# Optimization experiments

Measured on AMD Instinct MI355X. Metric: run time of the kernel, lower is better.

The kernel has to match this reference:

```python
import jax, jax.numpy as jnp
import numpy as np

B, Q, K, D, H = 2, 2048, 2048, 1024, 16
HD = D // H  # 64
EPS = 1e-6  # flax LayerNorm default epsilon


def setup_inputs() -> dict:
    key = jax.random.key(0)
    ks = jax.random.split(key, 12)
    s = 1.0 / np.sqrt(D)  # lecun_normal-like scale
    inputs_q = jax.random.normal(ks[0], (B, Q, D), jnp.float32)
    bias = jax.random.normal(ks[1], (B, 1, Q, K), jnp.float32)
    mask = jax.random.randint(ks[2], (B, 1, Q, K), 0, 2).astype(jnp.bool_)
    wq = jax.random.normal(ks[3], (D, H, HD), jnp.float32) * s
    wk = jax.random.normal(ks[4], (D, H, HD), jnp.float32) * s
    wv = jax.random.normal(ks[5], (D, H, HD), jnp.float32) * s
    bq = jnp.zeros((H, HD), jnp.float32)
    bk = jnp.zeros((H, HD), jnp.float32)
    bv = jnp.zeros((H, HD), jnp.float32)
    q_scale = jnp.ones((HD,), jnp.float32)
    k_scale = jnp.ones((HD,), jnp.float32)
    wo = jax.random.normal(ks[6], (H, HD, D), jnp.float32) * s
    bo = jnp.zeros((D,), jnp.float32)
    return dict(inputs_q=inputs_q, bias=bias, mask=mask, wq=wq, bq=bq,
                wk=wk, bk=bk, wv=wv, bv=bv, q_scale=q_scale, k_scale=k_scale,
                wo=wo, bo=bo)


def _layernorm_nobias(x, scale):
    # normalize over last axis (head_dim), no bias, like flax LayerNorm(use_bias=False)
    mean = jnp.mean(x, axis=-1, keepdims=True)
    var = jnp.mean(jnp.square(x - mean), axis=-1, keepdims=True)
    return (x - mean) * jax.lax.rsqrt(var + EPS) * scale


def reference(inputs_q, bias, mask, wq, bq, wk, bk, wv, bv, q_scale, k_scale, wo, bo):
    # QKV projections (self-attention: k and v inputs default to inputs_q)
    q = jnp.einsum('bqd,dhe->bqhe', inputs_q, wq) + bq  # [B,Q,H,HD]
    k = jnp.einsum('bkd,dhe->bkhe', inputs_q, wk) + bk  # [B,K,H,HD]
    v = jnp.einsum('bkd,dhe->bkhe', inputs_q, wv) + bv  # [B,K,H,HD]
    # optional QK layernorm (normalize_qk=True)
    q = _layernorm_nobias(q, q_scale)
    k = _layernorm_nobias(k, k_scale)
    # attention weights
    q = q / jnp.sqrt(jnp.asarray(q.shape[-1], q.dtype))
    attn = jnp.einsum('bqhe,bkhe->bhqk', q, k)  # [B,H,Q,K]
    attn = attn + bias
    big_neg = jnp.finfo(q.dtype).min
    attn = jnp.where(mask, attn, big_neg)
    attn = jax.nn.softmax(attn.astype(jnp.float32), axis=-1).astype(q.dtype)
    # weighted values + output projection
    x = jnp.einsum('bhqk,bkhe->bqhe', attn, v)  # [B,Q,H,HD]
    out = jnp.einsum('bqhe,heo->bqo', x, wo) + bo  # [B,Q,D]
    return out
```

## Files before the change

kernel.cpp:

```cpp
#include <hip/hip_runtime.h>
#include <cstdint>
#include <cstddef>

typedef __bf16 bf16_t;
typedef __bf16 bf16x8 __attribute__((ext_vector_type(8)));
typedef __bf16 bf16x4 __attribute__((ext_vector_type(4)));
typedef _Float16 f16_t;
typedef _Float16 f16x4 __attribute__((ext_vector_type(4)));
typedef float f32x4 __attribute__((ext_vector_type(4)));

constexpr int BB = 2, SS = 2048, DD = 1024, HH = 16, HDIM = 64;
constexpr int BS = BB * SS;
constexpr float LOG2E = 1.4426950408889634f;

__device__ __forceinline__ void glds16(const void* g, void* l) {
  __builtin_amdgcn_global_load_lds((const __attribute__((address_space(1))) void*)g,
                                   (__attribute__((address_space(3))) void*)l, 16, 0, 0);
}

__global__ __launch_bounds__(256) void prep_fused(
    const float* __restrict__ x, const float* __restrict__ wq, const float* __restrict__ wk,
    const float* __restrict__ wv, const float* __restrict__ wo, const float* __restrict__ bias,
    const int* __restrict__ mask, bf16_t* __restrict__ xb, bf16_t* __restrict__ wqkv_t,
    bf16_t* __restrict__ wo_t, bf16_t* __restrict__ bmq) {
  __shared__ float tile[64][65];
  int bid = blockIdx.x;
  int t = threadIdx.x;
  if (bid < 4096) {
    int i = bid * 256 + t;
    float4 v = ((const float4*)x)[i];
    union { bf16_t h[4]; uint2 u; } o;
    o.h[0] = (bf16_t)v.x; o.h[1] = (bf16_t)v.y; o.h[2] = (bf16_t)v.z; o.h[3] = (bf16_t)v.w;
    ((uint2*)xb)[i] = o.u;
  } else if (bid < 5120) {
    int id = bid - 4096;
    int which = id >> 8, tr = (id >> 4) & 15, tc = id & 15;
    const float* src = (which == 0) ? wq : (which == 1) ? wk : (which == 2) ? wv : wo;
    bf16_t* dst = (which < 3) ? wqkv_t : wo_t;
    int noff = (which < 3) ? which * 1024 : 0;
#pragma unroll
    for (int p = 0; p < 4; ++p) {
      int e = (p * 256 + t) * 4;
      int r = e >> 6, c = e & 63;
      float4 v = *(const float4*)&src[(size_t)(tr * 64 + r) * 1024 + tc * 64 + c];
      tile[r][c] = v.x; tile[r][c + 1] = v.y; tile[r][c + 2] = v.z; tile[r][c + 3] = v.w;
    }
    __syncthreads();
#pragma unroll
    for (int p = 0; p < 4; ++p) {
      int e = (p * 256 + t) * 4;
      int r = e >> 6, c = e & 63;
      union { bf16_t h[4]; uint2 u; } o;
#pragma unroll
      for (int j = 0; j < 4; ++j) o.h[j] = (bf16_t)tile[c + j][r];
      *(uint2*)&dst[(size_t)(noff + tc * 64 + r) * 1024 + tr * 64 + c] = o.u;
    }
  } else {
    int i = (bid - 5120) * 256 + t;
    float4 b0 = ((const float4*)bias)[i * 2];
    float4 b1 = ((const float4*)bias)[i * 2 + 1];
    int4 m0 = ((const int4*)mask)[i * 2];
    int4 m1 = ((const int4*)mask)[i * 2 + 1];
    union { bf16_t h[8]; uint4 u; } o;
    o.h[0] = (bf16_t)(m0.x ? b0.x * LOG2E - 8.0f : -2.0e38f);
    o.h[1] = (bf16_t)(m0.y ? b0.y * LOG2E - 8.0f : -2.0e38f);
    o.h[2] = (bf16_t)(m0.z ? b0.z * LOG2E - 8.0f : -2.0e38f);
    o.h[3] = (bf16_t)(m0.w ? b0.w * LOG2E - 8.0f : -2.0e38f);
    o.h[4] = (bf16_t)(m1.x ? b1.x * LOG2E - 8.0f : -2.0e38f);
    o.h[5] = (bf16_t)(m1.y ? b1.y * LOG2E - 8.0f : -2.0e38f);
    o.h[6] = (bf16_t)(m1.z ? b1.z * LOG2E - 8.0f : -2.0e38f);
    o.h[7] = (bf16_t)(m1.w ? b1.w * LOG2E - 8.0f : -2.0e38f);
    ((uint4*)bmq)[i] = o.u;
  }
}

template <bool OUT_F32>
__global__ __launch_bounds__(256) void gemm_bt(const bf16_t* __restrict__ A,
                                               const bf16_t* __restrict__ Bt,
                                               bf16_t* __restrict__ Cb, float* __restrict__ Cf,
                                               const float* __restrict__ bias, int M, int N,
                                               int Kd) {
  __shared__ __align__(16) bf16_t As[128][32];
  __shared__ __align__(16) bf16_t Bs[128][32];
  int tid = threadIdx.x;
  int lane = tid & 63, w = tid >> 6;
  int lo = lane & 15, quad = lane >> 4;
  int wm = w >> 1, wn = w & 1;
  int m0 = blockIdx.y * 128, n0 = blockIdx.x * 128;
  int srow = lane >> 2;
  int scol = (lane & 3) * 8;
  f32x4 acc[4][4] = {};
  for (int kk = 0; kk < Kd; kk += 32) {
#pragma unroll
    for (int t = 0; t < 2; ++t) {
      int rb = (w * 2 + t) * 16;
      glds16(&A[(size_t)(m0 + rb + srow) * Kd + kk + scol], &As[rb][0]);
      glds16(&Bt[(size_t)(n0 + rb + srow) * Kd + kk + scol], &Bs[rb][0]);
    }
    asm volatile("s_waitcnt vmcnt(0)" ::: "memory");
    __syncthreads();
    bf16x8 am[4], bn[4];
#pragma unroll
    for (int i = 0; i < 4; ++i) am[i] = *(const bf16x8*)&As[wm * 64 + i * 16 + lo][quad * 8];
#pragma unroll
    for (int i = 0; i < 4; ++i) bn[i] = *(const bf16x8*)&Bs[wn * 64 + i * 16 + lo][quad * 8];
#pragma unroll
    for (int mi = 0; mi < 4; ++mi)
#pragma unroll
      for (int ni = 0; ni < 4; ++ni)
        acc[mi][ni] = __builtin_amdgcn_mfma_f32_16x16x32_bf16(am[mi], bn[ni], acc[mi][ni], 0, 0, 0);
    __syncthreads();
  }
#pragma unroll
  for (int mi = 0; mi < 4; ++mi) {
#pragma unroll
    for (int ni = 0; ni < 4; ++ni) {
#pragma unroll
      for (int r = 0; r < 4; ++r) {
        int row = m0 + wm * 64 + mi * 16 + quad * 4 + r;
        int col = n0 + wn * 64 + ni * 16 + lo;
        float v = acc[mi][ni][r];
        if (OUT_F32)
          Cf[(size_t)row * N + col] = v + bias[col];
        else
          Cb[(size_t)row * N + col] = (bf16_t)v;
      }
    }
  }
}

__global__ __launch_bounds__(256) void postqkv(const bf16_t* __restrict__ Cqkv,
                                               const float* __restrict__ bq,
                                               const float* __restrict__ bk,
                                               const float* __restrict__ bv,
                                               const float* __restrict__ q_scale,
                                               const float* __restrict__ k_scale,
                                               bf16_t* __restrict__ qb, bf16_t* __restrict__ kb,
                                               f16_t* __restrict__ vt) {
  __shared__ float tile[64][65];
  int bid = blockIdx.x;
  int t = threadIdx.x;
  if (bid < 32768) {
    int mode = bid >> 14;
    int vec = (bid & 16383) * 4 + (t >> 6);
    int lane = t & 63;
    int bs = vec >> 4, h = vec & 15;
    int b = bs >> 11, s = bs & 2047;
    const float* badd = (mode == 0) ? bq : bk;
    float x = (float)Cqkv[(size_t)bs * 3072 + mode * 1024 + h * 64 + lane] + badd[h * 64 + lane];
    float sum = x;
#pragma unroll
    for (int off = 32; off >= 1; off >>= 1) sum += __shfl_xor(sum, off, 64);
    float mean = sum * (1.0f / 64.0f);
    float d = x - mean;
    float vs = d * d;
#pragma unroll
    for (int off = 32; off >= 1; off >>= 1) vs += __shfl_xor(vs, off, 64);
    float var = vs * (1.0f / 64.0f);
    const float* sc = (mode == 0) ? q_scale : k_scale;
    float y = d * rsqrtf(var + 1e-6f) * sc[lane];
    if (mode == 0) y *= 0.125f * LOG2E;
    bf16_t* dst = (mode == 0) ? qb : kb;
    dst[(size_t)((b * 16 + h) * 2048 + s) * 64 + lane] = (bf16_t)y;
  } else {
    int id2 = bid - 32768;
    int st = id2 & 31, h = (id2 >> 5) & 15, b = id2 >> 9;
#pragma unroll
    for (int p = 0; p < 2; ++p) {
      int e = (p * 256 + t) * 8;
      int r = e >> 6, c = e & 63;
      bf16x8 v8 = *(const bf16x8*)&Cqkv[(size_t)(b * SS + st * 64 + r) * 3072 + 2048 + h * 64 + c];
#pragma unroll
      for (int j = 0; j < 8; ++j) tile[r][c + j] = (float)v8[j] + bv[h * 64 + c + j];
    }
    __syncthreads();
#pragma unroll
    for (int p = 0; p < 2; ++p) {
      int e = (p * 256 + t) * 8;
      int r = e >> 6, c = e & 63;
      union { f16_t h[8]; uint4 u; } o;
#pragma unroll
      for (int j = 0; j < 8; ++j) o.h[j] = (f16_t)tile[c + j][r];
      *(uint4*)&vt[(size_t)((b * HH + h) * HDIM + r) * SS + st * 64 + c] = o.u;
    }
  }
}

__global__ __launch_bounds__(256) void attn_kernel(const bf16_t* __restrict__ qb,
                                                   const bf16_t* __restrict__ kb,
                                                   const f16_t* __restrict__ vt,
                                                   const bf16_t* __restrict__ bmq,
                                                   bf16_t* __restrict__ xout) {
  __shared__ __align__(16) bf16_t Ks[64][72];
  __shared__ __align__(16) f16_t Vs[64][72];
  __shared__ __align__(16) bf16_t Bm[128][72];
  int tid = threadIdx.x;
  int lane = tid & 63, w = tid >> 6;
  int lo = lane & 15, quad = lane >> 4;
  int qt = blockIdx.x, h = blockIdx.y, b = blockIdx.z;
  size_t headoff = (size_t)(b * HH + h) * SS * HDIM;
  int q0b = qt * 128;
  int q0 = q0b + w * 32;
  const bf16_t* kbase = kb + headoff;
  const f16_t* vbase = vt + headoff;
  const bf16_t* bmbase = bmq + (size_t)b * SS * SS;

  bf16x8 bqf[2][2];
#pragma unroll
  for (int qg = 0; qg < 2; ++qg)
#pragma unroll
    for (int ec = 0; ec < 2; ++ec)
      bqf[qg][ec] =
          *(const bf16x8*)&qb[headoff + (size_t)(q0 + qg * 16 + lo) * HDIM + ec * 32 + quad * 8];

  f16x4 ones;
#pragma unroll
  for (int j = 0; j < 4; ++j) ones[j] = (f16_t)1.0f;

  f32x4 ot[2][4] = {};
  f32x4 lacc[2] = {};

  for (int kt = 0; kt < SS / 64; ++kt) {
    int k0 = kt * 64;
#pragma unroll
    for (int p = 0; p < 2; ++p) {
      int idx = (p * 256 + tid) * 8;
      int r = idx >> 6, c = idx & 63;
      *(uint4*)&Ks[r][c] = *(const uint4*)&kbase[(size_t)(k0 + r) * HDIM + c];
      *(uint4*)&Vs[r][c] = *(const uint4*)&vbase[(size_t)r * SS + k0 + c];
    }
#pragma unroll
    for (int p = 0; p < 4; ++p) {
      int idx = (p * 256 + tid) * 8;
      int r = idx >> 6, c = idx & 63;
      *(uint4*)&Bm[r][c] = *(const uint4*)&bmbase[(size_t)(q0b + r) * SS + k0 + c];
    }
    __syncthreads();

    bf16x8 ka[4][2];
#pragma unroll
    for (int mb = 0; mb < 4; ++mb)
#pragma unroll
      for (int ec = 0; ec < 2; ++ec)
        ka[mb][ec] = *(const bf16x8*)&Ks[mb * 16 + lo][ec * 32 + quad * 8];

    f16x4 pf[2][4];
#pragma unroll
    for (int qg = 0; qg < 2; ++qg) {
#pragma unroll
      for (int mb = 0; mb < 4; ++mb) {
        bf16x4 bm4 = *(const bf16x4*)&Bm[w * 32 + qg * 16 + lo][mb * 16 + quad * 4];
        f32x4 s;
#pragma unroll
        for (int r = 0; r < 4; ++r) s[r] = (float)bm4[r];
        s = __builtin_amdgcn_mfma_f32_16x16x32_bf16(ka[mb][0], bqf[qg][0], s, 0, 0, 0);
        s = __builtin_amdgcn_mfma_f32_16x16x32_bf16(ka[mb][1], bqf[qg][1], s, 0, 0, 0);
#pragma unroll
        for (int r = 0; r < 4; ++r) pf[qg][mb][r] = (f16_t)__builtin_amdgcn_exp2f(s[r]);
      }
    }

#pragma unroll
    for (int mb = 0; mb < 4; ++mb) {
#pragma unroll
      for (int eb = 0; eb < 4; ++eb) {
        f16x4 va = *(const f16x4*)&Vs[eb * 16 + lo][mb * 16 + quad * 4];
#pragma unroll
        for (int qg = 0; qg < 2; ++qg)
          ot[qg][eb] = __builtin_amdgcn_mfma_f32_16x16x16f16(va, pf[qg][mb], ot[qg][eb], 0, 0, 0);
      }
#pragma unroll
      for (int qg = 0; qg < 2; ++qg)
        lacc[qg] = __builtin_amdgcn_mfma_f32_16x16x16f16(ones, pf[qg][mb], lacc[qg], 0, 0, 0);
    }
    __syncthreads();
  }

#pragma unroll
  for (int qg = 0; qg < 2; ++qg) {
    float rl = 1.0f / lacc[qg][0];
    int q = q0 + qg * 16 + lo;
#pragma unroll
    for (int eb = 0; eb < 4; ++eb) {
      union { bf16_t h4[4]; uint2 u; } o;
#pragma unroll
      for (int r = 0; r < 4; ++r) o.h4[r] = (bf16_t)(ot[qg][eb][r] * rl);
      *(uint2*)&xout[(size_t)(b * SS + q) * DD + h * 64 + eb * 16 + quad * 4] = o.u;
    }
  }
}

extern "C" void kernel_launch(void* const* d_in, const int* in_sizes, int n_in, void* d_out,
                              int out_size, void* d_ws, size_t ws_size, hipStream_t stream) {
  const float* inputs_q = (const float*)d_in[0];
  const float* bias = (const float*)d_in[1];
  const int* mask = (const int*)d_in[2];
  const float* wq = (const float*)d_in[3];
  const float* bq = (const float*)d_in[4];
  const float* wk = (const float*)d_in[5];
  const float* bk = (const float*)d_in[6];
  const float* wv = (const float*)d_in[7];
  const float* bv = (const float*)d_in[8];
  const float* q_scale = (const float*)d_in[9];
  const float* k_scale = (const float*)d_in[10];
  const float* wo = (const float*)d_in[11];
  const float* bo = (const float*)d_in[12];
  float* out = (float*)d_out;

  char* ws = (char*)d_ws;
  bf16_t* wo_t   = (bf16_t*)(ws);
  bf16_t* bmq    = (bf16_t*)(ws + ((size_t)2 << 20));
  bf16_t* cqkv   = (bf16_t*)(ws + ((size_t)19 << 20));
  bf16_t* xattn  = (bf16_t*)(ws + ((size_t)19 << 20));
  bf16_t* xb     = (bf16_t*)(ws + ((size_t)43 << 20));
  bf16_t* qb2    = (bf16_t*)(ws + ((size_t)43 << 20));
  bf16_t* wqkv_t = (bf16_t*)(ws + ((size_t)51 << 20));
  bf16_t* kb2    = (bf16_t*)(ws + ((size_t)51 << 20));
  f16_t*  vtb    = (f16_t*)(ws + ((size_t)59 << 20));

  prep_fused<<<9216, 256, 0, stream>>>(inputs_q, wq, wk, wv, wo, bias, mask, xb, wqkv_t, wo_t, bmq);
  gemm_bt<false><<<dim3(24, 32), 256, 0, stream>>>(xb, wqkv_t, cqkv, nullptr, nullptr, BS, 3072, DD);
  postqkv<<<33792, 256, 0, stream>>>(cqkv, bq, bk, bv, q_scale, k_scale, qb2, kb2, vtb);
  attn_kernel<<<dim3(SS / 128, HH, BB), 256, 0, stream>>>(qb2, kb2, vtb, bmq, xattn);
  gemm_bt<true><<<dim3(8, 32), 256, 0, stream>>>(xattn, wo_t, nullptr, out, bo, BS, 1024, DD);
}
```

Baseline: 300.7 us.

## Fuse QKV bias and QK layernorm into GEMM epilogue, widen K tile

The QKV GEMM epilogue now adds biases, applies the Q/K layernorm with shuffle reductions across the 64-wide head slice, and writes Q/K directly in head-major bf16 layout and V as f16. A much smaller kernel then only transposes V. This removes the separate postqkv pass and its round trip of the full QKV intermediate through memory. The GEMM K-step is also doubled to 64 to halve the barrier count, at the cost of more LDS per block. Variance is now computed in one pass as E[x²]−mean², which can be slightly less accurate.

```diff
diff --git a/kernel.cpp b/kernel.cpp
--- a/kernel.cpp
+++ b/kernel.cpp
@@ -74,115 +74,128 @@
   }
 }
 
-template <bool OUT_F32>
-__global__ __launch_bounds__(256) void gemm_bt(const bf16_t* __restrict__ A,
-                                               const bf16_t* __restrict__ Bt,
-                                               bf16_t* __restrict__ Cb, float* __restrict__ Cf,
-                                               const float* __restrict__ bias, int M, int N,
-                                               int Kd) {
-  __shared__ __align__(16) bf16_t As[128][32];
-  __shared__ __align__(16) bf16_t Bs[128][32];
+template <int MODE>
+__global__ __launch_bounds__(256) void gemm_bt(
+    const bf16_t* __restrict__ A, const bf16_t* __restrict__ Bt, float* __restrict__ Cf,
+    const float* __restrict__ bias, bf16_t* __restrict__ qbo, bf16_t* __restrict__ kbo,
+    f16_t* __restrict__ cvo, const float* __restrict__ bq, const float* __restrict__ bk,
+    const float* __restrict__ bv, const float* __restrict__ qs, const float* __restrict__ ks,
+    int M, int N, int Kd) {
+  __shared__ __align__(16) bf16_t As[128][64];
+  __shared__ __align__(16) bf16_t Bs[128][64];
   int tid = threadIdx.x;
   int lane = tid & 63, w = tid >> 6;
   int lo = lane & 15, quad = lane >> 4;
   int wm = w >> 1, wn = w & 1;
   int m0 = blockIdx.y * 128, n0 = blockIdx.x * 128;
-  int srow = lane >> 2;
-  int scol = (lane & 3) * 8;
+  int srow = lane >> 3;
+  int scol = (lane & 7) * 8;
   f32x4 acc[4][4] = {};
-  for (int kk = 0; kk < Kd; kk += 32) {
-#pragma unroll
-    for (int t = 0; t < 2; ++t) {
-      int rb = (w * 2 + t) * 16;
+  for (int kk = 0; kk < Kd; kk += 64) {
+#pragma unroll
+    for (int t = 0; t < 4; ++t) {
+      int rb = (w * 4 + t) * 8;
       glds16(&A[(size_t)(m0 + rb + srow) * Kd + kk + scol], &As[rb][0]);
       glds16(&Bt[(size_t)(n0 + rb + srow) * Kd + kk + scol], &Bs[rb][0]);
     }
     asm volatile("s_waitcnt vmcnt(0)" ::: "memory");
     __syncthreads();
-    bf16x8 am[4], bn[4];
-#pragma unroll
-    for (int i = 0; i < 4; ++i) am[i] = *(const bf16x8*)&As[wm * 64 + i * 16 + lo][quad * 8];
-#pragma unroll
-    for (int i = 0; i < 4; ++i) bn[i] = *(const bf16x8*)&Bs[wn * 64 + i * 16 + lo][quad * 8];
+#pragma unroll
+    for (int kc = 0; kc < 2; ++kc) {
+      bf16x8 am[4], bn[4];
+#pragma unroll
+      for (int i = 0; i < 4; ++i)
+        am[i] = *(const bf16x8*)&As[wm * 64 + i * 16 + lo][kc * 32 + quad * 8];
+#pragma unroll
+      for (int i = 0; i < 4; ++i)
+        bn[i] = *(const bf16x8*)&Bs[wn * 64 + i * 16 + lo][kc * 32 + quad * 8];
+#pragma unroll
+      for (int mi = 0; mi < 4; ++mi)
+#pragma unroll
+        for (int ni = 0; ni < 4; ++ni)
+          acc[mi][ni] = __builtin_amdgcn_mfma_f32_16x16x32_bf16(am[mi], bn[ni], acc[mi][ni], 0, 0, 0);
+    }
+    __syncthreads();
+  }
+
+  if (MODE == 0) {
 #pragma unroll
     for (int mi = 0; mi < 4; ++mi)
 #pragma unroll
       for (int ni = 0; ni < 4; ++ni)
-        acc[mi][ni] = __builtin_amdgcn_mfma_f32_16x16x32_bf16(am[mi], bn[ni], acc[mi][ni], 0, 0, 0);
-    __syncthreads();
-  }
-#pragma unroll
-  for (int mi = 0; mi < 4; ++mi) {
-#pragma unroll
-    for (int ni = 0; ni < 4; ++ni) {
+#pragma unroll
+        for (int r = 0; r < 4; ++r) {
+          int row = m0 + wm * 64 + mi * 16 + quad * 4 + r;
+          int col = n0 + wn * 64 + ni * 16 + lo;
+          Cf[(size_t)row * N + col] = acc[mi][ni][r] + bias[col];
+        }
+  } else {
+    int sec = blockIdx.x >> 3;
+    int hh = ((blockIdx.x & 7) << 1) + wn;
+    const float* badd = (sec == 0) ? bq : (sec == 1) ? bk : bv;
+    float bia[4], scv[4];
+#pragma unroll
+    for (int ni = 0; ni < 4; ++ni) bia[ni] = badd[hh * 64 + ni * 16 + lo];
+    if (sec < 2) {
+      const float* scp = (sec == 0) ? qs : ks;
+#pragma unroll
+      for (int ni = 0; ni < 4; ++ni) scv[ni] = scp[ni * 16 + lo];
+    }
+#pragma unroll
+    for (int mi = 0; mi < 4; ++mi) {
 #pragma unroll
       for (int r = 0; r < 4; ++r) {
-        int row = m0 + wm * 64 + mi * 16 + quad * 4 + r;
-        int col = n0 + wn * 64 + ni * 16 + lo;
-        float v = acc[mi][ni][r];
-        if (OUT_F32)
-          Cf[(size_t)row * N + col] = v + bias[col];
-        else
-          Cb[(size_t)row * N + col] = (bf16_t)v;
+        float x[4];
+#pragma unroll
+        for (int ni = 0; ni < 4; ++ni) x[ni] = acc[mi][ni][r] + bia[ni];
+        int bs = m0 + wm * 64 + mi * 16 + quad * 4 + r;
+        if (sec < 2) {
+          float s1 = x[0] + x[1] + x[2] + x[3];
+          float s2 = x[0] * x[0] + x[1] * x[1] + x[2] * x[2] + x[3] * x[3];
+#pragma unroll
+          for (int off = 8; off >= 1; off >>= 1) {
+            s1 += __shfl_xor(s1, off, 64);
+            s2 += __shfl_xor(s2, off, 64);
+          }
+          float mean = s1 * (1.0f / 64.0f);
+          float var = s2 * (1.0f / 64.0f) - mean * mean;
+          float inv = rsqrtf(fmaxf(var, 0.0f) + 1e-6f);
+          float mul = inv * ((sec == 0) ? 0.125f * LOG2E : 1.0f);
+          bf16_t* dst = ((sec == 0) ? qbo : kbo) +
+                        ((size_t)(((bs >> 11) << 4) + hh) * 2048 + (bs & 2047)) * 64;
+#pragma unroll
+          for (int ni = 0; ni < 4; ++ni)
+            dst[ni * 16 + lo] = (bf16_t)((x[ni] - mean) * mul * scv[ni]);
+        } else {
+          f16_t* dst = cvo + (size_t)bs * 1024 + hh * 64;
+#pragma unroll
+          for (int ni = 0; ni < 4; ++ni) dst[ni * 16 + lo] = (f16_t)x[ni];
+        }
       }
     }
   }
 }
 
-__global__ __launch_bounds__(256) void postqkv(const bf16_t* __restrict__ Cqkv,
-                                               const float* __restrict__ bq,
-                                               const float* __restrict__ bk,
-                                               const float* __restrict__ bv,
-                                               const float* __restrict__ q_scale,
-                                               const float* __restrict__ k_scale,
-                                               bf16_t* __restrict__ qb, bf16_t* __restrict__ kb,
-                                               f16_t* __restrict__ vt) {
-  __shared__ float tile[64][65];
-  int bid = blockIdx.x;
+__global__ __launch_bounds__(256) void vt_small(const f16_t* __restrict__ cv,
+                                                f16_t* __restrict__ vt) {
+  __shared__ f16_t tile[64][72];
+  int st = blockIdx.x, h = blockIdx.y, b = blockIdx.z;
   int t = threadIdx.x;
-  if (bid < 32768) {
-    int mode = bid >> 14;
-    int vec = (bid & 16383) * 4 + (t >> 6);
-    int lane = t & 63;
-    int bs = vec >> 4, h = vec & 15;
-    int b = bs >> 11, s = bs & 2047;
-    const float* badd = (mode == 0) ? bq : bk;
-    float x = (float)Cqkv[(size_t)bs * 3072 + mode * 1024 + h * 64 + lane] + badd[h * 64 + lane];
-    float sum = x;
-#pragma unroll
-    for (int off = 32; off >= 1; off >>= 1) sum += __shfl_xor(sum, off, 64);
-    float mean = sum * (1.0f / 64.0f);
-    float d = x - mean;
-    float vs = d * d;
-#pragma unroll
-    for (int off = 32; off >= 1; off >>= 1) vs += __shfl_xor(vs, off, 64);
-    float var = vs * (1.0f / 64.0f);
-    const float* sc = (mode == 0) ? q_scale : k_scale;
-    float y = d * rsqrtf(var + 1e-6f) * sc[lane];
-    if (mode == 0) y *= 0.125f * LOG2E;
-    bf16_t* dst = (mode == 0) ? qb : kb;
-    dst[(size_t)((b * 16 + h) * 2048 + s) * 64 + lane] = (bf16_t)y;
-  } else {
-    int id2 = bid - 32768;
-    int st = id2 & 31, h = (id2 >> 5) & 15, b = id2 >> 9;
-#pragma unroll
-    for (int p = 0; p < 2; ++p) {
-      int e = (p * 256 + t) * 8;
-      int r = e >> 6, c = e & 63;
-      bf16x8 v8 = *(const bf16x8*)&Cqkv[(size_t)(b * SS + st * 64 + r) * 3072 + 2048 + h * 64 + c];
-#pragma unroll
-      for (int j = 0; j < 8; ++j) tile[r][c + j] = (float)v8[j] + bv[h * 64 + c + j];
-    }
-    __syncthreads();
-#pragma unroll
-    for (int p = 0; p < 2; ++p) {
-      int e = (p * 256 + t) * 8;
-      int r = e >> 6, c = e & 63;
-      union { f16_t h[8]; uint4 u; } o;
-#pragma unroll
-      for (int j = 0; j < 8; ++j) o.h[j] = (f16_t)tile[c + j][r];
-      *(uint4*)&vt[(size_t)((b * HH + h) * HDIM + r) * SS + st * 64 + c] = o.u;
-    }
+#pragma unroll
+  for (int p = 0; p < 2; ++p) {
+    int e = (p * 256 + t) * 8;
+    int r = e >> 6, c = e & 63;
+    *(uint4*)&tile[r][c] = *(const uint4*)&cv[(size_t)(b * SS + st * 64 + r) * 1024 + h * 64 + c];
+  }
+  __syncthreads();
+#pragma unroll
+  for (int p = 0; p < 2; ++p) {
+    int e = (p * 256 + t) * 8;
+    int r = e >> 6, c = e & 63;
+    union { f16_t h[8]; uint4 u; } o;
+#pragma unroll
+    for (int j = 0; j < 8; ++j) o.h[j] = tile[c + j][r];
+    *(uint4*)&vt[(size_t)((b * HH + h) * HDIM + r) * SS + st * 64 + c] = o.u;
   }
 }
 
@@ -310,17 +323,20 @@
   char* ws = (char*)d_ws;
   bf16_t* wo_t   = (bf16_t*)(ws);
   bf16_t* bmq    = (bf16_t*)(ws + ((size_t)2 << 20));
-  bf16_t* cqkv   = (bf16_t*)(ws + ((size_t)19 << 20));
-  bf16_t* xattn  = (bf16_t*)(ws + ((size_t)19 << 20));
+  bf16_t* qb2    = (bf16_t*)(ws + ((size_t)19 << 20));
+  bf16_t* kb2    = (bf16_t*)(ws + ((size_t)27 << 20));
+  f16_t*  cv     = (f16_t*)(ws + ((size_t)35 << 20));
+  bf16_t* xattn  = (bf16_t*)(ws + ((size_t)35 << 20));
   bf16_t* xb     = (bf16_t*)(ws + ((size_t)43 << 20));
-  bf16_t* qb2    = (bf16_t*)(ws + ((size_t)43 << 20));
+  f16_t*  vtb    = (f16_t*)(ws + ((size_t)43 << 20));
   bf16_t* wqkv_t = (bf16_t*)(ws + ((size_t)51 << 20));
-  bf16_t* kb2    = (bf16_t*)(ws + ((size_t)51 << 20));
-  f16_t*  vtb    = (f16_t*)(ws + ((size_t)59 << 20));
 
   prep_fused<<<9216, 256, 0, stream>>>(inputs_q, wq, wk, wv, wo, bias, mask, xb, wqkv_t, wo_t, bmq);
-  gemm_bt<false><<<dim3(24, 32), 256, 0, stream>>>(xb, wqkv_t, cqkv, nullptr, nullptr, BS, 3072, DD);
-  postqkv<<<33792, 256, 0, stream>>>(cqkv, bq, bk, bv, q_scale, k_scale, qb2, kb2, vtb);
+  gemm_bt<2><<<dim3(24, 32), 256, 0, stream>>>(xb, wqkv_t, nullptr, nullptr, qb2, kb2, cv, bq, bk,
+                                               bv, q_scale, k_scale, BS, 3072, DD);
+  vt_small<<<dim3(32, 16, 2), 256, 0, stream>>>(cv, vtb);
   attn_kernel<<<dim3(SS / 128, HH, BB), 256, 0, stream>>>(qb2, kb2, vtb, bmq, xattn);
-  gemm_bt<true><<<dim3(8, 32), 256, 0, stream>>>(xattn, wo_t, nullptr, out, bo, BS, 1024, DD);
-}
+  gemm_bt<0><<<dim3(8, 32), 256, 0, stream>>>(xattn, wo_t, out, bo, nullptr, nullptr, nullptr,
+                                              nullptr, nullptr, nullptr, nullptr, nullptr, BS,
+                                              1024, DD);
+}
```

Result: no change. 301.1 us (+0.1%).
